# Optimization experiments

Hardware: AMD Instinct MI355X
Metric: run time of the kernel (lower is better)

The kernel has to match this reference:

```python
import jax, jax.numpy as jnp
import numpy as np

B, N, D, S = 4, 8, 64, 8192  # batch, heads, dim_head, seq_len


def setup_inputs() -> dict:
    key = jax.random.key(0)
    kq, kk, kv = jax.random.split(key, 3)
    q = jax.random.normal(kq, (B, N, D, S), dtype=jnp.float32)
    k = jax.random.normal(kk, (B, N, D, S), dtype=jnp.float32)
    v = jax.random.normal(kv, (B, N, D, S), dtype=jnp.float32)
    return {"q": q, "k": k, "v": v}


def reference(q, k, v):
    # q, k, v: [b, n, d, s] = [batch, heads, dim_head, seq]
    scale = q.shape[-2] ** -0.5  # dim_head^-0.5
    qs = jax.nn.softmax(q, axis=-2) * scale   # softmax over feature dim
    ks = jax.nn.softmax(k, axis=-1)           # softmax over seq dim
    # kv context: [b, n, d, d] -- avoids the O(s^2) score matrix
    context = jnp.einsum('bnis,bnjs->bnij', ks, v)
    # out: [b, n, d, s]
    return jnp.einsum('bnij,bnis->bnjs', context, qs)
```

## Files before the change

### kernel.cpp

```cpp
#include <hip/hip_runtime.h>
#include <math.h>


typedef _Float16 half8 __attribute__((ext_vector_type(8)));
typedef float floatx4 __attribute__((ext_vector_type(4)));

constexpr int BHEADS = 32;
constexpr int DH     = 64;
constexpr int SEQ    = 8192;
constexpr int NCHUNK = 16;
constexpr float QSCALE = 0.125f;

__global__ __launch_bounds__(256)
void ctx_partial_kernel(const float* __restrict__ K, const float* __restrict__ V,
                        float* __restrict__ partial, float* __restrict__ Zp)
{
    const int head  = blockIdx.y;
    const int chunk = blockIdx.x;
    const int t     = threadIdx.x;
    const int lane  = t & 63;
    const int w     = t >> 6;
    const int ln    = lane & 15;
    const int q8    = lane >> 4;

    const float* kh = K + (size_t)head * DH * SEQ;
    const float* vh = V + (size_t)head * DH * SEQ;

    __shared__ __align__(16) _Float16 et[64 * 72];
    __shared__ __align__(16) _Float16 vt[64 * 72];
    __shared__ __align__(16) float zred[64 * 8];

    const int r0 = t >> 3;
    const int c0 = 8 * (t & 7);
    const int s_blk = chunk * 512;

    float4 pk[2][2], pv[2][2];
    #pragma unroll
    for (int rr = 0; rr < 2; ++rr) {
        const size_t base = (size_t)(r0 + 32 * rr) * SEQ + s_blk + c0;
        pk[rr][0] = *(const float4*)(kh + base);
        pk[rr][1] = *(const float4*)(kh + base + 4);
        pv[rr][0] = *(const float4*)(vh + base);
        pv[rr][1] = *(const float4*)(vh + base + 4);
    }

    floatx4 acc[4];
    #pragma unroll
    for (int jt = 0; jt < 4; ++jt) acc[jt] = (floatx4){0.f, 0.f, 0.f, 0.f};
    float zacc[2] = {0.f, 0.f};

    for (int ts = 0; ts < 8; ++ts) {
        #pragma unroll
        for (int rr = 0; rr < 2; ++rr) {
            const int row = r0 + 32 * rr;
            float e[8];
            e[0] = __expf(pk[rr][0].x); e[1] = __expf(pk[rr][0].y);
            e[2] = __expf(pk[rr][0].z); e[3] = __expf(pk[rr][0].w);
            e[4] = __expf(pk[rr][1].x); e[5] = __expf(pk[rr][1].y);
            e[6] = __expf(pk[rr][1].z); e[7] = __expf(pk[rr][1].w);
            zacc[rr] += e[0]+e[1]+e[2]+e[3]+e[4]+e[5]+e[6]+e[7];
            half8 he, hv;
            #pragma unroll
            for (int x = 0; x < 4; ++x) {
                he[x] = (_Float16)e[x]; he[x+4] = (_Float16)e[x+4];
            }
            hv[0] = (_Float16)pv[rr][0].x; hv[1] = (_Float16)pv[rr][0].y;
            hv[2] = (_Float16)pv[rr][0].z; hv[3] = (_Float16)pv[rr][0].w;
            hv[4] = (_Float16)pv[rr][1].x; hv[5] = (_Float16)pv[rr][1].y;
            hv[6] = (_Float16)pv[rr][1].z; hv[7] = (_Float16)pv[rr][1].w;
            *(half8*)(et + row * 72 + c0) = he;
            *(half8*)(vt + row * 72 + c0) = hv;
        }
        __syncthreads();
        if (ts < 7) {
            #pragma unroll
            for (int rr = 0; rr < 2; ++rr) {
                const size_t base = (size_t)(r0 + 32 * rr) * SEQ + s_blk
                                    + (ts + 1) * 64 + c0;
                pk[rr][0] = *(const float4*)(kh + base);
                pk[rr][1] = *(const float4*)(kh + base + 4);
                pv[rr][0] = *(const float4*)(vh + base);
                pv[rr][1] = *(const float4*)(vh + base + 4);
            }
        }
        #pragma unroll
        for (int st = 0; st < 2; ++st) {
            const half8 a = *(const half8*)(et + (16 * w + ln) * 72 + st * 32 + q8 * 8);
            #pragma unroll
            for (int jt = 0; jt < 4; ++jt) {
                const half8 b = *(const half8*)(vt + (16 * jt + ln) * 72 + st * 32 + q8 * 8);
                acc[jt] = __builtin_amdgcn_mfma_f32_16x16x32_f16(a, b, acc[jt], 0, 0, 0);
            }
        }
        __syncthreads();
    }

    float* ph = partial + (size_t)(head * NCHUNK + chunk) * DH * DH;
    #pragma unroll
    for (int jt = 0; jt < 4; ++jt) {
        #pragma unroll
        for (int rr = 0; rr < 4; ++rr) {
            const int i = 16 * w + q8 * 4 + rr;
            const int j = 16 * jt + ln;
            ph[i * DH + j] = acc[jt][rr];
        }
    }
    zred[r0 * 8 + (t & 7)] = zacc[0];
    zred[(r0 + 32) * 8 + (t & 7)] = zacc[1];
    __syncthreads();
    if (t < 64) {
        const float4 z0 = *(const float4*)(zred + t * 8);
        const float4 z1 = *(const float4*)(zred + t * 8 + 4);
        Zp[(head * NCHUNK + chunk) * DH + t] =
            z0.x + z0.y + z0.z + z0.w + z1.x + z1.y + z1.z + z1.w;
    }
}

__global__ __launch_bounds__(256)
void reduce_kernel(const float* __restrict__ partial, const float* __restrict__ Zp,
                   _Float16* __restrict__ czT)
{
    const int h = blockIdx.x;
    const int t = threadIdx.x;
    __shared__ float rz[64];

    if (t < 64) {
        float z = 0.f;
        #pragma unroll
        for (int c = 0; c < NCHUNK; ++c)
            z += Zp[(h * NCHUNK + c) * DH + t];
        rz[t] = 1.0f / z;
    }
    __syncthreads();

    const float* ph = partial + (size_t)h * NCHUNK * DH * DH;
    _Float16* ct = czT + (size_t)h * DH * DH;
    #pragma unroll
    for (int rep = 0; rep < 4; ++rep) {
        const int idx = t + 256 * rep;
        const int i   = idx >> 4;
        const int j4  = idx & 15;
        float4 sum = {0.f, 0.f, 0.f, 0.f};
        #pragma unroll
        for (int c = 0; c < NCHUNK; ++c) {
            const float4 p = *(const float4*)(ph + (size_t)c * DH * DH + i * DH + j4 * 4);
            sum.x += p.x; sum.y += p.y; sum.z += p.z; sum.w += p.w;
        }
        const float r = rz[i];
        ct[(j4 * 4 + 0) * DH + i] = (_Float16)(sum.x * r);
        ct[(j4 * 4 + 1) * DH + i] = (_Float16)(sum.y * r);
        ct[(j4 * 4 + 2) * DH + i] = (_Float16)(sum.z * r);
        ct[(j4 * 4 + 3) * DH + i] = (_Float16)(sum.w * r);
    }
}

__global__ __launch_bounds__(256)
void out_kernel(const float* __restrict__ Q, const _Float16* __restrict__ czT,
                float* __restrict__ out)
{
    const int head = blockIdx.y;
    const int sb   = blockIdx.x;
    const int t    = threadIdx.x;
    const int lane = t & 63;
    const int w    = t >> 6;
    const int ln   = lane & 15;
    const int q8   = lane >> 4;

    __shared__ __align__(16) float    qf[64 * 68];
    __shared__ __align__(16) _Float16 eqT[64 * 64];
    __shared__ __align__(16) float    wred[64 * 4];

    const float* qh = Q + (size_t)head * DH * SEQ;
    const int r0 = t >> 4;
    const int sc = 4 * (t & 15);
    const int s0 = sb * 256;

    float4 pq[4];
    #pragma unroll
    for (int p = 0; p < 4; ++p)
        pq[p] = *(const float4*)(qh + (size_t)(r0 + 16 * p) * SEQ + s0 + sc);

    const _Float16* ch = czT + (size_t)head * DH * DH;
    const half8 a0 = *(const half8*)(ch + (16 * w + ln) * DH + 0  + q8 * 8);
    const half8 a1 = *(const half8*)(ch + (16 * w + ln) * DH + 32 + q8 * 8);

    for (int r = 0; r < 4; ++r) {
        #pragma unroll
        for (int p = 0; p < 4; ++p)
            *(float4*)(qf + (r0 + 16 * p) * 68 + sc) = pq[p];
        __syncthreads();
        {
            const int s  = t & 63;
            const int cg = t >> 6;
            float wsum = 0.f;
            #pragma unroll
            for (int h2 = 0; h2 < 2; ++h2) {
                const int cc = cg + 4 * h2;
                half8 p8;
                #pragma unroll
                for (int jj = 0; jj < 8; ++jj) {
                    const float e = __expf(qf[(8 * cc + jj) * 68 + s]);
                    wsum += e;
                    p8[jj] = (_Float16)e;
                }
                *(half8*)(eqT + s * 64 + ((cc ^ (s & 7)) * 8)) = p8;
            }
            wred[s * 4 + cg] = wsum;
        }
        if (r < 3) {
            #pragma unroll
            for (int p = 0; p < 4; ++p)
                pq[p] = *(const float4*)(qh + (size_t)(r0 + 16 * p) * SEQ
                                         + s0 + (r + 1) * 64 + sc);
        }
        __syncthreads();
        float rw[4];
        #pragma unroll
        for (int nt = 0; nt < 4; ++nt) {
            const int s2 = 16 * nt + ln;
            const float4 wv = *(const float4*)(wred + s2 * 4);
            rw[nt] = QSCALE / (wv.x + wv.y + wv.z + wv.w);
        }
        floatx4 acc[4];
        #pragma unroll
        for (int nt = 0; nt < 4; ++nt) acc[nt] = (floatx4){0.f, 0.f, 0.f, 0.f};
        #pragma unroll
        for (int st = 0; st < 2; ++st) {
            const half8 a = (st == 0) ? a0 : a1;
            #pragma unroll
            for (int nt = 0; nt < 4; ++nt) {
                const int s2 = 16 * nt + ln;
                const int cc = st * 4 + q8;
                const half8 b = *(const half8*)(eqT + s2 * 64 + ((cc ^ (s2 & 7)) * 8));
                acc[nt] = __builtin_amdgcn_mfma_f32_16x16x32_f16(a, b, acc[nt], 0, 0, 0);
            }
        }
        float* oh = out + (size_t)head * DH * SEQ + s0 + r * 64;
        #pragma unroll
        for (int nt = 0; nt < 4; ++nt) {
            const int s2 = 16 * nt + ln;
            #pragma unroll
            for (int rr = 0; rr < 4; ++rr) {
                const int j = 16 * w + q8 * 4 + rr;
                oh[(size_t)j * SEQ + s2] = acc[nt][rr] * rw[nt];
            }
        }
    }
}

extern "C" void kernel_launch(void* const* d_in, const int* in_sizes, int n_in,
                              void* d_out, int out_size, void* d_ws, size_t ws_size,
                              hipStream_t stream)
{
    const float* q = (const float*)d_in[0];
    const float* k = (const float*)d_in[1];
    const float* v = (const float*)d_in[2];
    float* out = (float*)d_out;

    float*    partial = (float*)d_ws;
    float*    Zp      = partial + BHEADS * NCHUNK * DH * DH;
    _Float16* czT     = (_Float16*)(Zp + BHEADS * NCHUNK * DH);

    ctx_partial_kernel<<<dim3(NCHUNK, BHEADS), 256, 0, stream>>>(k, v, partial, Zp);
    reduce_kernel<<<BHEADS, 256, 0, stream>>>(partial, Zp, czT);
    out_kernel<<<dim3(32, BHEADS), 256, 0, stream>>>(q, czT, out);
}
```

Baseline: 238.7 us.

## Increase grid parallelism across all kernels and use 32x32 MFMA in output

Doubles the number of sequence chunks in the context kernel and splits the reduce kernel four ways per head. It also halves the per-block sequence span in the output kernel. The output kernel now uses 32x32x16 MFMA tiles, with each wave covering a 32x32 output block, and the Q prefetch is moved earlier. The intent is better latency hiding and GPU occupancy. The cost is a larger partial-context buffer and more reduction traffic.

```diff
diff --git a/kernel.cpp b/kernel.cpp
--- a/kernel.cpp
+++ b/kernel.cpp
@@ -4,11 +4,12 @@
 
 typedef _Float16 half8 __attribute__((ext_vector_type(8)));
 typedef float floatx4 __attribute__((ext_vector_type(4)));
+typedef float floatx16 __attribute__((ext_vector_type(16)));
 
 constexpr int BHEADS = 32;
 constexpr int DH     = 64;
 constexpr int SEQ    = 8192;
-constexpr int NCHUNK = 16;
+constexpr int NCHUNK = 32;
 constexpr float QSCALE = 0.125f;
 
 __global__ __launch_bounds__(256)
@@ -32,7 +33,7 @@
 
     const int r0 = t >> 3;
     const int c0 = 8 * (t & 7);
-    const int s_blk = chunk * 512;
+    const int s_blk = chunk * 256;
 
     float4 pk[2][2], pv[2][2];
     #pragma unroll
@@ -49,7 +50,7 @@
     for (int jt = 0; jt < 4; ++jt) acc[jt] = (floatx4){0.f, 0.f, 0.f, 0.f};
     float zacc[2] = {0.f, 0.f};
 
-    for (int ts = 0; ts < 8; ++ts) {
+    for (int ts = 0; ts < 4; ++ts) {
         #pragma unroll
         for (int rr = 0; rr < 2; ++rr) {
             const int row = r0 + 32 * rr;
@@ -71,8 +72,7 @@
             *(half8*)(et + row * 72 + c0) = he;
             *(half8*)(vt + row * 72 + c0) = hv;
         }
-        __syncthreads();
-        if (ts < 7) {
+        if (ts < 3) {
             #pragma unroll
             for (int rr = 0; rr < 2; ++rr) {
                 const size_t base = (size_t)(r0 + 32 * rr) * SEQ + s_blk
@@ -83,6 +83,7 @@
                 pv[rr][1] = *(const float4*)(vh + base + 4);
             }
         }
+        __syncthreads();
         #pragma unroll
         for (int st = 0; st < 2; ++st) {
             const half8 a = *(const half8*)(et + (16 * w + ln) * 72 + st * 32 + q8 * 8);
@@ -120,38 +121,36 @@
 void reduce_kernel(const float* __restrict__ partial, const float* __restrict__ Zp,
                    _Float16* __restrict__ czT)
 {
-    const int h = blockIdx.x;
-    const int t = threadIdx.x;
-    __shared__ float rz[64];
-
-    if (t < 64) {
+    const int h  = blockIdx.x >> 2;
+    const int iq = blockIdx.x & 3;
+    const int t  = threadIdx.x;
+    __shared__ float rz[16];
+
+    if (t < 16) {
         float z = 0.f;
         #pragma unroll
         for (int c = 0; c < NCHUNK; ++c)
-            z += Zp[(h * NCHUNK + c) * DH + t];
+            z += Zp[(h * NCHUNK + c) * DH + 16 * iq + t];
         rz[t] = 1.0f / z;
     }
     __syncthreads();
 
+    const int il = t >> 4;
+    const int j4 = t & 15;
+    const int i  = 16 * iq + il;
     const float* ph = partial + (size_t)h * NCHUNK * DH * DH;
+    float4 sum = {0.f, 0.f, 0.f, 0.f};
+    #pragma unroll
+    for (int c = 0; c < NCHUNK; ++c) {
+        const float4 p = *(const float4*)(ph + (size_t)c * DH * DH + i * DH + j4 * 4);
+        sum.x += p.x; sum.y += p.y; sum.z += p.z; sum.w += p.w;
+    }
+    const float r = rz[il];
     _Float16* ct = czT + (size_t)h * DH * DH;
-    #pragma unroll
-    for (int rep = 0; rep < 4; ++rep) {
-        const int idx = t + 256 * rep;
-        const int i   = idx >> 4;
-        const int j4  = idx & 15;
-        float4 sum = {0.f, 0.f, 0.f, 0.f};
-        #pragma unroll
-        for (int c = 0; c < NCHUNK; ++c) {
-            const float4 p = *(const float4*)(ph + (size_t)c * DH * DH + i * DH + j4 * 4);
-            sum.x += p.x; sum.y += p.y; sum.z += p.z; sum.w += p.w;
-        }
-        const float r = rz[i];
-        ct[(j4 * 4 + 0) * DH + i] = (_Float16)(sum.x * r);
-        ct[(j4 * 4 + 1) * DH + i] = (_Float16)(sum.y * r);
-        ct[(j4 * 4 + 2) * DH + i] = (_Float16)(sum.z * r);
-        ct[(j4 * 4 + 3) * DH + i] = (_Float16)(sum.w * r);
-    }
+    ct[(j4 * 4 + 0) * DH + i] = (_Float16)(sum.x * r);
+    ct[(j4 * 4 + 1) * DH + i] = (_Float16)(sum.y * r);
+    ct[(j4 * 4 + 2) * DH + i] = (_Float16)(sum.z * r);
+    ct[(j4 * 4 + 3) * DH + i] = (_Float16)(sum.w * r);
 }
 
 __global__ __launch_bounds__(256)
@@ -163,8 +162,10 @@
     const int t    = threadIdx.x;
     const int lane = t & 63;
     const int w    = t >> 6;
-    const int ln   = lane & 15;
-    const int q8   = lane >> 4;
+    const int l31  = lane & 31;
+    const int lh   = lane >> 5;
+    const int jw   = 32 * (w & 1);
+    const int sw   = 32 * (w >> 1);
 
     __shared__ __align__(16) float    qf[64 * 68];
     __shared__ __align__(16) _Float16 eqT[64 * 64];
@@ -173,7 +174,7 @@
     const float* qh = Q + (size_t)head * DH * SEQ;
     const int r0 = t >> 4;
     const int sc = 4 * (t & 15);
-    const int s0 = sb * 256;
+    const int s0 = sb * 128;
 
     float4 pq[4];
     #pragma unroll
@@ -181,13 +182,21 @@
         pq[p] = *(const float4*)(qh + (size_t)(r0 + 16 * p) * SEQ + s0 + sc);
 
     const _Float16* ch = czT + (size_t)head * DH * DH;
-    const half8 a0 = *(const half8*)(ch + (16 * w + ln) * DH + 0  + q8 * 8);
-    const half8 a1 = *(const half8*)(ch + (16 * w + ln) * DH + 32 + q8 * 8);
-
-    for (int r = 0; r < 4; ++r) {
+    half8 afr[4];
+    #pragma unroll
+    for (int st = 0; st < 4; ++st)
+        afr[st] = *(const half8*)(ch + (jw + l31) * DH + st * 16 + lh * 8);
+
+    for (int r = 0; r < 2; ++r) {
         #pragma unroll
         for (int p = 0; p < 4; ++p)
             *(float4*)(qf + (r0 + 16 * p) * 68 + sc) = pq[p];
+        if (r < 1) {
+            #pragma unroll
+            for (int p = 0; p < 4; ++p)
+                pq[p] = *(const float4*)(qh + (size_t)(r0 + 16 * p) * SEQ
+                                         + s0 + 64 + sc);
+        }
         __syncthreads();
         {
             const int s  = t & 63;
@@ -207,43 +216,22 @@
             }
             wred[s * 4 + cg] = wsum;
         }
-        if (r < 3) {
-            #pragma unroll
-            for (int p = 0; p < 4; ++p)
-                pq[p] = *(const float4*)(qh + (size_t)(r0 + 16 * p) * SEQ
-                                         + s0 + (r + 1) * 64 + sc);
-        }
-        __syncthreads();
-        float rw[4];
-        #pragma unroll
-        for (int nt = 0; nt < 4; ++nt) {
-            const int s2 = 16 * nt + ln;
-            const float4 wv = *(const float4*)(wred + s2 * 4);
-            rw[nt] = QSCALE / (wv.x + wv.y + wv.z + wv.w);
-        }
-        floatx4 acc[4];
-        #pragma unroll
-        for (int nt = 0; nt < 4; ++nt) acc[nt] = (floatx4){0.f, 0.f, 0.f, 0.f};
-        #pragma unroll
-        for (int st = 0; st < 2; ++st) {
-            const half8 a = (st == 0) ? a0 : a1;
-            #pragma unroll
-            for (int nt = 0; nt < 4; ++nt) {
-                const int s2 = 16 * nt + ln;
-                const int cc = st * 4 + q8;
-                const half8 b = *(const half8*)(eqT + s2 * 64 + ((cc ^ (s2 & 7)) * 8));
-                acc[nt] = __builtin_amdgcn_mfma_f32_16x16x32_f16(a, b, acc[nt], 0, 0, 0);
-            }
+        __syncthreads();
+        const float4 wv = *(const float4*)(wred + (sw + l31) * 4);
+        const float rw = QSCALE / (wv.x + wv.y + wv.z + wv.w);
+        floatx16 acc = {};
+        #pragma unroll
+        for (int st = 0; st < 4; ++st) {
+            const int s2 = sw + l31;
+            const int cc = 2 * st + lh;
+            const half8 b = *(const half8*)(eqT + s2 * 64 + ((cc ^ (s2 & 7)) * 8));
+            acc = __builtin_amdgcn_mfma_f32_32x32x16_f16(afr[st], b, acc, 0, 0, 0);
         }
         float* oh = out + (size_t)head * DH * SEQ + s0 + r * 64;
         #pragma unroll
-        for (int nt = 0; nt < 4; ++nt) {
-            const int s2 = 16 * nt + ln;
-            #pragma unroll
-            for (int rr = 0; rr < 4; ++rr) {
-                const int j = 16 * w + q8 * 4 + rr;
-                oh[(size_t)j * SEQ + s2] = acc[nt][rr] * rw[nt];
-            }
+        for (int rg = 0; rg < 16; ++rg) {
+            const int j = jw + (rg & 3) + 8 * (rg >> 2) + 4 * lh;
+            oh[(size_t)j * SEQ + sw + l31] = acc[rg] * rw;
         }
     }
 }
@@ -262,6 +250,6 @@
     _Float16* czT     = (_Float16*)(Zp + BHEADS * NCHUNK * DH);
 
     ctx_partial_kernel<<<dim3(NCHUNK, BHEADS), 256, 0, stream>>>(k, v, partial, Zp);
-    reduce_kernel<<<BHEADS, 256, 0, stream>>>(partial, Zp, czT);
-    out_kernel<<<dim3(32, BHEADS), 256, 0, stream>>>(q, czT, out);
-}
+    reduce_kernel<<<BHEADS * 4, 256, 0, stream>>>(partial, Zp, czT);
+    out_kernel<<<dim3(64, BHEADS), 256, 0, stream>>>(q, czT, out);
+}
```

Measured after the change: 235.4 us. No clear change (-1.4%).
